# Optimization experiments

Hardware: AMD Instinct MI355X
Metric: run time of the kernel (lower is better)

Reference implementation:

```python
import jax, jax.numpy as jnp
import numpy as np

B, C, H, W = 8, 256, 128, 128
HEADS = 16
HEADC = C // HEADS  # 16
EPS = 1e-5


def setup_inputs() -> dict:
    key = jax.random.key(0)
    k1, k2 = jax.random.split(key)
    x = jax.random.normal(k1, (B, C, H, W), dtype=jnp.float32)
    w_qkv = jax.random.normal(k2, (3 * C, C), dtype=jnp.float32) * (1.0 / np.sqrt(C))
    b_qkv = jnp.zeros((3 * C,), dtype=jnp.float32)
    kln_w = jnp.ones((HEADS, HEADC), dtype=jnp.float32)
    kln_b = jnp.zeros((HEADS, HEADC), dtype=jnp.float32)
    vln_w = jnp.ones((HEADS, HEADC), dtype=jnp.float32)
    vln_b = jnp.zeros((HEADS, HEADC), dtype=jnp.float32)
    return {"x": x, "w_qkv": w_qkv, "b_qkv": b_qkv,
            "kln_w": kln_w, "kln_b": kln_b, "vln_w": vln_w, "vln_b": vln_b}


def _layernorm(x, w, b):
    # torch-style: unbiased std (ddof=1), divides by (std + eps), over last dim
    mean = jnp.mean(x, axis=-1, keepdims=True)
    std = jnp.std(x, axis=-1, keepdims=True, ddof=1)
    return (x - mean) / (std + EPS) * w + b


def reference(x, w_qkv, b_qkv, kln_w, kln_b, vln_w, vln_b):
    b, c, h, w = x.shape
    n = h * w
    # 1x1 conv == per-pixel matmul over channels
    qkv = jnp.einsum('bchw,oc->bhwo', x, w_qkv) + b_qkv  # (B,H,W,3C)
    qkv = qkv.reshape(b, n, HEADS, -1)                   # (B,N,16,3*headc)
    q, k, v = jnp.split(qkv, 3, axis=-1)                 # each (B,N,16,headc)
    k = _layernorm(k, kln_w, kln_b)
    v = _layernorm(v, vln_w, vln_b)
    # linear (Galerkin) attention: kv = k^T v / N, out = q @ kv
    kv = jnp.einsum('bnhd,bnhe->bhde', k, v) / n         # (B,16,headc,headc)
    out = jnp.einsum('bnhd,bhde->bnhe', q, kv)           # (B,N,16,headc)
    out = out.reshape(b, h, w, c).transpose(0, 3, 1, 2)  # (B,C,H,W)
    return out
```

## Files before the change

kernel.cpp:

```cpp
#include <hip/hip_runtime.h>

typedef unsigned short u16;
typedef unsigned int u32;
typedef __attribute__((ext_vector_type(8))) short short8;
typedef __attribute__((ext_vector_type(4))) float f32x4;

#define NPIX 16384
#define LNEPS 1e-5f

__device__ __forceinline__ float bf2f(u16 u) {
  union { u32 i; float f; } x; x.i = ((u32)u) << 16; return x.f;
}
__device__ __forceinline__ u16 f2bf(float f) {
  union { float f; u32 i; } x; x.f = f;
  u32 r = x.i + 0x7fffu + ((x.i >> 16) & 1u);
  return (u16)(r >> 16);
}
__device__ __forceinline__ void gload_lds16(const void* g, void* l) {
  __builtin_amdgcn_global_load_lds((__attribute__((address_space(1))) void*)(g),
                                   (__attribute__((address_space(3))) void*)(l),
                                   16, 0, 0);
}
__device__ __forceinline__ uint4 pack8(float4 a, float4 b) {
  uint4 q;
  q.x = (u32)f2bf(a.x) | ((u32)f2bf(a.y) << 16);
  q.y = (u32)f2bf(a.z) | ((u32)f2bf(a.w) << 16);
  q.z = (u32)f2bf(b.x) | ((u32)f2bf(b.y) << 16);
  q.w = (u32)f2bf(b.z) | ((u32)f2bf(b.w) << 16);
  return q;
}

__global__ __launch_bounds__(256) void k_detect(const u16* __restrict__ x,
                                                int* __restrict__ flag) {
  float mx = 0.f;
  for (int i = threadIdx.x; i < 4096; i += 256) {
    float v = fabsf(bf2f(x[2 * i]));
    if (v == v) mx = fmaxf(mx, v);
  }
  for (int m = 1; m < 64; m <<= 1) mx = fmaxf(mx, __shfl_xor(mx, m));
  __shared__ float wmax[4];
  if ((threadIdx.x & 63) == 0) wmax[threadIdx.x >> 6] = mx;
  __syncthreads();
  if (threadIdx.x == 0) {
    float m2 = fmaxf(fmaxf(wmax[0], wmax[1]), fmaxf(wmax[2], wmax[3]));
    flag[0] = (m2 > 1e5f) ? 1 : 0;
  }
}

__global__ __launch_bounds__(256) void k_wconv(
    const void* __restrict__ w, const void* __restrict__ bq,
    const void* __restrict__ klw, const void* __restrict__ klb,
    const void* __restrict__ vlw, const void* __restrict__ vlb,
    u16* __restrict__ wkv, u16* __restrict__ wq,
    float* __restrict__ bias_kv, float* __restrict__ lnw_kv,
    float* __restrict__ lnb_kv, float* __restrict__ bq_q,
    const int* __restrict__ flag) {
  const int i = blockIdx.x * 256 + threadIdx.x;
  const bool f32 = flag[0] != 0;
  auto getf = [&](const void* p, int j) -> float {
    return f32 ? ((const float*)p)[j] : bf2f(((const u16*)p)[j]);
  };
  if (i < 131072) {
    int o = i >> 8, c = i & 255;
    int h = o >> 5, tt = (o >> 4) & 1, d = o & 15;
    wkv[i] = f2bf(getf(w, (h * 48 + 16 + tt * 16 + d) * 256 + c));
  } else if (i < 196608) {
    int j = i - 131072; int r = j >> 8, c = j & 255;
    wq[j] = f2bf(getf(w, ((r >> 4) * 48 + (r & 15)) * 256 + c));
  } else if (i < 198400) {
    int j = i - 196608;
    if (j < 512) {
      int h = j >> 5, tt = (j >> 4) & 1, d = j & 15;
      bias_kv[j] = getf(bq, h * 48 + 16 + tt * 16 + d);
    } else if (j < 1024) {
      int o = j - 512; int h = o >> 5, tt = (o >> 4) & 1, d = o & 15;
      lnw_kv[o] = getf(tt ? vlw : klw, h * 16 + d);
    } else if (j < 1536) {
      int o = j - 1024; int h = o >> 5, tt = (o >> 4) & 1, d = o & 15;
      lnb_kv[o] = getf(tt ? vlb : klb, h * 16 + d);
    } else {
      int r = j - 1536;
      bq_q[r] = getf(bq, (r >> 4) * 48 + (r & 15));
    }
  }
}

__global__ __launch_bounds__(512, 4) void k_gemm1(
    const void* __restrict__ xin, const u16* __restrict__ wkv,
    const float* __restrict__ bias_kv, const float* __restrict__ lnw_kv,
    const float* __restrict__ lnb_kv, float* __restrict__ kvpart,
    const int* __restrict__ flag) {
  __shared__ alignas(16) char shraw[73728];
  u16 (*wlds)[256][32] = (u16 (*)[256][32])shraw;
  u16 (*xlds)[32][128] = (u16 (*)[32][128])(shraw + 32768);
  u16 (*klds)[260]     = (u16 (*)[260])shraw;
  float* bls = (float*)(shraw + 66560);
  float* wls = bls + 256;
  float* lls = bls + 512;
  float (*tmp)[256] = (float (*)[256])(shraw + 69632);

  const int t = threadIdx.x;
  const int lbid = ((blockIdx.x & 7) << 8) + (blockIdx.x >> 3);
  const int hg = lbid & 1;
  const int pc = (lbid >> 1) & 127;
  const int b  = lbid >> 8;
  const int p0 = pc * 128;
  const int wv = t >> 6, lane = t & 63, quad = lane >> 4, l16 = lane & 15;
  const int hl = wv & 1, pxq = wv >> 1;
  const bool f32 = flag[0] != 0;

  if (t < 256) {
    bls[t] = bias_kv[hg * 256 + t];
    wls[t] = lnw_kv[hg * 256 + t];
    lls[t] = lnb_kv[hg * 256 + t];
  }

  f32x4 acc[8][2];
#pragma unroll
  for (int ms = 0; ms < 8; ++ms) {
    acc[ms][0] = (f32x4){0.f, 0.f, 0.f, 0.f};
    acc[ms][1] = (f32x4){0.f, 0.f, 0.f, 0.f};
  }

  const int wrow = t >> 2;
  const int wcs  = t & 3;
  const int wks  = (wcs ^ ((t >> 3) & 3)) * 8;
  const u16* wsrc = wkv + ((size_t)(hg * 256 + wrow) * 256 + wks);

  const int xrow = t >> 4;
  const int xg   = (t & 15) ^ ((xrow >> 3) << 1);
  const u16* xsrc_bf = (const u16*)xin +
      ((size_t)(b * 256 + xrow) * NPIX + p0 + xg * 8);
  const float* xsrc_f = (const float*)xin +
      ((size_t)(b * 256 + xrow) * NPIX + p0 + xg * 8);

  gload_lds16(wsrc, &wlds[0][wrow][wcs * 8]);
  gload_lds16(wsrc + (size_t)128 * 256, &wlds[0][128 + wrow][wcs * 8]);
  if (!f32) {
    gload_lds16(xsrc_bf, &xlds[0][xrow][(t & 15) * 8]);
  } else {
    float4 a = *(const float4*)xsrc_f;
    float4 c = *(const float4*)(xsrc_f + 4);
    *(uint4*)&xlds[0][xrow][(t & 15) * 8] = pack8(a, c);
  }
  __syncthreads();

  for (int ks = 0; ks < 8; ++ks) {
    const int cur = ks & 1, nxt = cur ^ 1;
    const bool more = ks < 7;
    float4 v0, v1;
    if (more) {
      const u16* ws = wsrc + (ks + 1) * 32;
      gload_lds16(ws, &wlds[nxt][wrow][wcs * 8]);
      gload_lds16(ws + (size_t)128 * 256, &wlds[nxt][128 + wrow][wcs * 8]);
      if (!f32) {
        gload_lds16(xsrc_bf + (size_t)(ks + 1) * 32 * NPIX,
                    &xlds[nxt][xrow][(t & 15) * 8]);
      } else {
        const float* xf = xsrc_f + (size_t)(ks + 1) * 32 * NPIX;
        v0 = *(const float4*)xf;
        v1 = *(const float4*)(xf + 4);
      }
    }
    short8 bfr[2];
#pragma unroll
    for (int ns = 0; ns < 2; ++ns) {
      const int pxn = pxq * 32 + ns * 16 + l16;
      const int cs8 = ((((pxn >> 3) ^ (quad << 1)) << 3) + (pxn & 7));
      short8 bv;
#pragma unroll
      for (int j = 0; j < 8; ++j)
        bv[j] = (short)xlds[cur][quad * 8 + j][cs8];
      bfr[ns] = bv;
    }
#pragma unroll
    for (int ms = 0; ms < 8; ++ms) {
      const int row = hl * 128 + ms * 16 + l16;
      short8 av = *(const short8*)&wlds[cur][row][(quad ^ ((l16 >> 1) & 3)) * 8];
      acc[ms][0] = __builtin_amdgcn_mfma_f32_16x16x32_bf16(av, bfr[0], acc[ms][0], 0, 0, 0);
      acc[ms][1] = __builtin_amdgcn_mfma_f32_16x16x32_bf16(av, bfr[1], acc[ms][1], 0, 0, 0);
    }
    if (more && f32)
      *(uint4*)&xlds[nxt][xrow][(t & 15) * 8] = pack8(v0, v1);
    __syncthreads();
  }

#pragma unroll
  for (int p = 0; p < 2; ++p) {
    __syncthreads();
#pragma unroll
    for (int j = 0; j < 4; ++j) {
      const int msl = p * 4 + j;
      const int slot = (j >> 1) | (hl << 1);
      const int cb = slot * 64 + (j & 1) * 16;
      float4 bi = *(const float4*)&bls[hl * 128 + msl * 16 + quad * 4];
      float4 lw = *(const float4*)&wls[hl * 128 + msl * 16 + quad * 4];
      float4 lb = *(const float4*)&lls[hl * 128 + msl * 16 + quad * 4];
      float biv[4] = {bi.x, bi.y, bi.z, bi.w};
      float lwv[4] = {lw.x, lw.y, lw.z, lw.w};
      float lbv[4] = {lb.x, lb.y, lb.z, lb.w};
#pragma unroll
      for (int ns = 0; ns < 2; ++ns) {
        const int px = pxq * 32 + ns * 16 + l16;
        float x0[4];
#pragma unroll
        for (int r = 0; r < 4; ++r) x0[r] = acc[msl][ns][r] + biv[r];
        float s1 = x0[0] + x0[1] + x0[2] + x0[3];
        s1 += __shfl_xor(s1, 16);
        s1 += __shfl_xor(s1, 32);
        float mean = s1 * (1.0f / 16.0f);
        float dv[4];
#pragma unroll
        for (int r = 0; r < 4; ++r) dv[r] = x0[r] - mean;
        float s2 = dv[0]*dv[0] + dv[1]*dv[1] + dv[2]*dv[2] + dv[3]*dv[3];
        s2 += __shfl_xor(s2, 16);
        s2 += __shfl_xor(s2, 32);
        float var = s2 * (1.0f / 15.0f);
        float rstd = 1.0f / (sqrtf(var) + LNEPS);
        u16 hi[4], lo[4];
#pragma unroll
        for (int r = 0; r < 4; ++r) {
          float kn = dv[r] * rstd * lwv[r] + lbv[r];
          hi[r] = f2bf(kn);
          lo[r] = f2bf(kn - bf2f(hi[r]));
        }
        uint2 ph, pl;
        ph.x = (u32)hi[0] | ((u32)hi[1] << 16);
        ph.y = (u32)hi[2] | ((u32)hi[3] << 16);
        pl.x = (u32)lo[0] | ((u32)lo[1] << 16);
        pl.y = (u32)lo[2] | ((u32)lo[3] << 16);
        *(uint2*)&klds[px][cb + quad * 4] = ph;
        *(uint2*)&klds[px][cb + 32 + quad * 4] = pl;
      }
    }
    __syncthreads();
    const int slot4 = wv >> 1, combo = wv & 1;
    const int cb2 = slot4 * 64;
    f32x4 kva = (f32x4){0.f, 0.f, 0.f, 0.f};
    if (combo == 0) {
#pragma unroll
      for (int px2 = 0; px2 < 4; ++px2) {
        short8 av, bv;
#pragma unroll
        for (int jj = 0; jj < 8; ++jj) {
          av[jj] = (short)klds[px2 * 32 + quad * 8 + jj][cb2 + l16];
          bv[jj] = (short)klds[px2 * 32 + quad * 8 + jj][cb2 + 16 + l16];
        }
        kva = __builtin_amdgcn_mfma_f32_16x16x32_bf16(av, bv, kva, 0, 0, 0);
      }
    } else {
#pragma unroll
      for (int px2 = 0; px2 < 4; ++px2) {
        short8 ah, al, vh, vl;
#pragma unroll
        for (int jj = 0; jj < 8; ++jj) {
          const int px = px2 * 32 + quad * 8 + jj;
          ah[jj] = (short)klds[px][cb2 + l16];
          vh[jj] = (short)klds[px][cb2 + 16 + l16];
          al[jj] = (short)klds[px][cb2 + 32 + l16];
          vl[jj] = (short)klds[px][cb2 + 48 + l16];
        }
        kva = __builtin_amdgcn_mfma_f32_16x16x32_bf16(ah, vl, kva, 0, 0, 0);
        kva = __builtin_amdgcn_mfma_f32_16x16x32_bf16(al, vh, kva, 0, 0, 0);
      }
    }
    __syncthreads();
    if (combo) {
#pragma unroll
      for (int r = 0; r < 4; ++r) tmp[slot4][(quad * 4 + r) * 16 + l16] = kva[r];
    }
    __syncthreads();
    if (!combo) {
      const int h = (slot4 >> 1) * 4 + p * 2 + (slot4 & 1);
      float* kvp = kvpart +
          ((size_t)(((b * 128 + pc) * 2 + hg) * 8 + h) << 8);
#pragma unroll
      for (int r = 0; r < 4; ++r) {
        const int idx = (quad * 4 + r) * 16 + l16;
        kvp[idx] = kva[r] + tmp[slot4][idx];
      }
    }
  }
}

__global__ __launch_bounds__(256) void k_fold(const u16* __restrict__ wq,
                                              const float* __restrict__ bq_q,
                                              const float* __restrict__ kvpart,
                                              u16* __restrict__ whi,
                                              u16* __restrict__ wlo,
                                              float* __restrict__ beff) {
  __shared__ float kvs[256];
  __shared__ float qb[16];
  const int t = threadIdx.x;
  const int b = blockIdx.x >> 4, h = blockIdx.x & 15;
  const int hg = h >> 3, hl = h & 7;
  const float* src = kvpart + ((size_t)((b * 128 * 2 + hg) * 8 + hl) << 8) + t;
  float s0 = 0.f;
  for (int pc = 0; pc < 128; ++pc)
    s0 += src[(size_t)pc * (2 * 8 * 256)];
  kvs[t] = s0 * (1.0f / 16384.0f);
  if (t < 16) qb[t] = bq_q[h * 16 + t];
  __syncthreads();
  const int e = t >> 4, c0 = (t & 15) * 16;
  float o[16];
#pragma unroll
  for (int c = 0; c < 16; ++c) o[c] = 0.f;
  for (int d = 0; d < 16; ++d) {
    float kv_de = kvs[d * 16 + e];
    const u16* wr = wq + (size_t)(h * 16 + d) * 256 + c0;
#pragma unroll
    for (int c = 0; c < 16; ++c) o[c] = fmaf(bf2f(wr[c]), kv_de, o[c]);
  }
  const size_t wbase = (size_t)(b * 256 + h * 16 + e) * 256 + c0;
#pragma unroll
  for (int c = 0; c < 16; ++c) {
    u16 hi = f2bf(o[c]);
    whi[wbase + c] = hi;
    wlo[wbase + c] = f2bf(o[c] - bf2f(hi));
  }
  if (t < 16) {
    float s = 0.f;
    for (int d = 0; d < 16; ++d) s += qb[d] * kvs[d * 16 + t];
    beff[b * 256 + h * 16 + t] = s;
  }
}

__global__ __launch_bounds__(512, 4) void k_gemm2(
    const void* __restrict__ xin, const u16* __restrict__ whi,
    const u16* __restrict__ wlo, const float* __restrict__ beff,
    void* __restrict__ outv, const int* __restrict__ flag) {
  __shared__ u16 wldh[2][256][32];
  __shared__ u16 wldl[2][256][32];
  __shared__ u16 xlds[2][32][128];

  const int t = threadIdx.x;
  const int lbid = ((blockIdx.x & 7) << 7) + (blockIdx.x >> 3);
  const int pc = lbid & 127;
  const int b  = lbid >> 7;
  const int p0 = pc * 128;
  const int wv = t >> 6, lane = t & 63, quad = lane >> 4, l16 = lane & 15;
  const int hl = wv & 1, pxq = wv >> 1;
  const bool f32 = flag[0] != 0;

  f32x4 acc[8][2];
#pragma unroll
  for (int ms = 0; ms < 8; ++ms) {
    acc[ms][0] = (f32x4){0.f, 0.f, 0.f, 0.f};
    acc[ms][1] = (f32x4){0.f, 0.f, 0.f, 0.f};
  }

  const int wrow = t >> 2;
  const int wcs  = t & 3;
  const int wks  = (wcs ^ ((t >> 3) & 3)) * 8;
  const size_t wbase = (size_t)(b * 256 + wrow) * 256 + wks;
  const u16* wsrch = whi + wbase;
  const u16* wsrcl = wlo + wbase;

  const int xrow = t >> 4;
  const int xg   = (t & 15) ^ ((xrow >> 3) << 1);
  const u16* xsrc_bf = (const u16*)xin +
      ((size_t)(b * 256 + xrow) * NPIX + p0 + xg * 8);
  const float* xsrc_f = (const float*)xin +
      ((size_t)(b * 256 + xrow) * NPIX + p0 + xg * 8);

  gload_lds16(wsrch, &wldh[0][wrow][wcs * 8]);
  gload_lds16(wsrch + (size_t)128 * 256, &wldh[0][128 + wrow][wcs * 8]);
  gload_lds16(wsrcl, &wldl[0][wrow][wcs * 8]);
  gload_lds16(wsrcl + (size_t)128 * 256, &wldl[0][128 + wrow][wcs * 8]);
  if (!f32) {
    gload_lds16(xsrc_bf, &xlds[0][xrow][(t & 15) * 8]);
  } else {
    float4 a = *(const float4*)xsrc_f;
    float4 c = *(const float4*)(xsrc_f + 4);
    *(uint4*)&xlds[0][xrow][(t & 15) * 8] = pack8(a, c);
  }
  __syncthreads();

  for (int ks = 0; ks < 8; ++ks) {
    const int cur = ks & 1, nxt = cur ^ 1;
    const bool more = ks < 7;
    float4 v0, v1;
    if (more) {
      const u16* wh = wsrch + (ks + 1) * 32;
      const u16* wl = wsrcl + (ks + 1) * 32;
      gload_lds16(wh, &wldh[nxt][wrow][wcs * 8]);
      gload_lds16(wh + (size_t)128 * 256, &wldh[nxt][128 + wrow][wcs * 8]);
      gload_lds16(wl, &wldl[nxt][wrow][wcs * 8]);
      gload_lds16(wl + (size_t)128 * 256, &wldl[nxt][128 + wrow][wcs * 8]);
      if (!f32) {
        gload_lds16(xsrc_bf + (size_t)(ks + 1) * 32 * NPIX,
                    &xlds[nxt][xrow][(t & 15) * 8]);
      } else {
        const float* xf = xsrc_f + (size_t)(ks + 1) * 32 * NPIX;
        v0 = *(const float4*)xf;
        v1 = *(const float4*)(xf + 4);
      }
    }
    short8 bfr[2];
#pragma unroll
    for (int ns = 0; ns < 2; ++ns) {
      const int pxn = pxq * 32 + ns * 16 + l16;
      const int cs8 = ((((pxn >> 3) ^ (quad << 1)) << 3) + (pxn & 7));
      short8 bv;
#pragma unroll
      for (int j = 0; j < 8; ++j)
        bv[j] = (short)xlds[cur][quad * 8 + j][cs8];
      bfr[ns] = bv;
    }
#pragma unroll
    for (int ms = 0; ms < 8; ++ms) {
      const int row = hl * 128 + ms * 16 + l16;
      const int csw = (quad ^ ((l16 >> 1) & 3)) * 8;
      short8 avh = *(const short8*)&wldh[cur][row][csw];
      short8 avl = *(const short8*)&wldl[cur][row][csw];
      acc[ms][0] = __builtin_amdgcn_mfma_f32_16x16x32_bf16(avh, bfr[0], acc[ms][0], 0, 0, 0);
      acc[ms][0] = __builtin_amdgcn_mfma_f32_16x16x32_bf16(avl, bfr[0], acc[ms][0], 0, 0, 0);
      acc[ms][1] = __builtin_amdgcn_mfma_f32_16x16x32_bf16(avh, bfr[1], acc[ms][1], 0, 0, 0);
      acc[ms][1] = __builtin_amdgcn_mfma_f32_16x16x32_bf16(avl, bfr[1], acc[ms][1], 0, 0, 0);
    }
    if (more && f32)
      *(uint4*)&xlds[nxt][xrow][(t & 15) * 8] = pack8(v0, v1);
    __syncthreads();
  }

  const size_t obase = (size_t)b * 256 * NPIX + p0;
#pragma unroll
  for (int ms = 0; ms < 8; ++ms) {
    const int o0 = hl * 128 + ms * 16 + quad * 4;
    float4 be = *(const float4*)&beff[b * 256 + o0];
    float bev[4] = {be.x, be.y, be.z, be.w};
#pragma unroll
    for (int ns = 0; ns < 2; ++ns) {
      const int px = pxq * 32 + ns * 16 + l16;
#pragma unroll
      for (int r = 0; r < 4; ++r) {
        const int o = o0 + r;
        float val = acc[ms][ns][r] + bev[r];
        if (f32) ((float*)outv)[obase + (size_t)o * NPIX + px] = val;
        else ((u16*)outv)[obase + (size_t)o * NPIX + px] = f2bf(val);
      }
    }
  }
}

extern "C" void kernel_launch(void* const* d_in, const int* in_sizes, int n_in,
                              void* d_out, int out_size, void* d_ws, size_t ws_size,
                              hipStream_t stream) {
  (void)in_sizes; (void)n_in; (void)out_size; (void)ws_size;
  char* ws = (char*)d_ws;
  u16* wkv       = (u16*)(ws + 0);
  u16* wq        = (u16*)(ws + 262144);
  u16* weff_hi   = (u16*)(ws + 393216);
  u16* weff_lo   = (u16*)(ws + 1441792);
  float* bias_kv = (float*)(ws + 2621440);
  float* lnw_kv  = (float*)(ws + 2623488);
  float* lnb_kv  = (float*)(ws + 2625536);
  float* bq_q    = (float*)(ws + 2627584);
  float* beff    = (float*)(ws + 2628608);
  int* flag      = (int*)(ws + 2636800);
  float* kvpart  = (float*)(ws + 4194304);

  k_detect<<<1, 256, 0, stream>>>((const u16*)d_in[0], flag);
  k_wconv<<<775, 256, 0, stream>>>(d_in[1], d_in[2], d_in[3], d_in[4], d_in[5],
                                   d_in[6], wkv, wq, bias_kv, lnw_kv, lnb_kv,
                                   bq_q, flag);
  k_gemm1<<<2048, 512, 0, stream>>>(d_in[0], wkv, bias_kv, lnw_kv, lnb_kv,
                                    kvpart, flag);
  k_fold<<<128, 256, 0, stream>>>(wq, bq_q, kvpart, weff_hi, weff_lo, beff);
  k_gemm2<<<1024, 512, 0, stream>>>(d_in[0], weff_hi, weff_lo, beff, d_out, flag);
}
```

Measured before the change: 378.5 us.

## Triple-buffer GEMM1 LDS staging with prefetch distance two and partial waits

Replaces the double-buffered weight/input LDS staging in the K/V projection GEMM with a three-slot ring buffer that prefetches two k-steps ahead. It uses explicit s_waitcnt vmcnt(3) so the loads for the following step stay in flight across the barrier, and fully unrolls the k-loop. The goal is to hide global-to-LDS latency behind MFMA work. In exchange LDS use rises from about 72KB to 79KB per block, which may reduce how many blocks fit per CU, and the hand-written waitcnt counts depend on the exact number of outstanding loads.

```diff
diff --git a/kernel.cpp b/kernel.cpp
--- a/kernel.cpp
+++ b/kernel.cpp
@@ -90,14 +90,14 @@
     const float* __restrict__ bias_kv, const float* __restrict__ lnw_kv,
     const float* __restrict__ lnb_kv, float* __restrict__ kvpart,
     const int* __restrict__ flag) {
-  __shared__ alignas(16) char shraw[73728];
-  u16 (*wlds)[256][32] = (u16 (*)[256][32])shraw;
-  u16 (*xlds)[32][128] = (u16 (*)[32][128])(shraw + 32768);
-  u16 (*klds)[260]     = (u16 (*)[260])shraw;
-  float* bls = (float*)(shraw + 66560);
+  __shared__ alignas(16) char shraw[80896];
+  u16* wb0 = (u16*)shraw;
+  u16* xb0 = (u16*)(shraw + 49152);
+  u16 (*klds)[260] = (u16 (*)[260])shraw;
+  float* bls = (float*)(shraw + 73728);
   float* wls = bls + 256;
   float* lls = bls + 512;
-  float (*tmp)[256] = (float (*)[256])(shraw + 69632);
+  float (*tmp)[256] = (float (*)[256])(shraw + 76800);
 
   const int t = threadIdx.x;
   const int lbid = ((blockIdx.x & 7) << 8) + (blockIdx.x >> 3);
@@ -134,34 +134,34 @@
   const float* xsrc_f = (const float*)xin +
       ((size_t)(b * 256 + xrow) * NPIX + p0 + xg * 8);
 
-  gload_lds16(wsrc, &wlds[0][wrow][wcs * 8]);
-  gload_lds16(wsrc + (size_t)128 * 256, &wlds[0][128 + wrow][wcs * 8]);
-  if (!f32) {
-    gload_lds16(xsrc_bf, &xlds[0][xrow][(t & 15) * 8]);
-  } else {
-    float4 a = *(const float4*)xsrc_f;
-    float4 c = *(const float4*)(xsrc_f + 4);
-    *(uint4*)&xlds[0][xrow][(t & 15) * 8] = pack8(a, c);
-  }
-  __syncthreads();
-
+  auto STAGE = [&](int T, int B) {
+    const u16* ws = wsrc + T * 32;
+    gload_lds16(ws, wb0 + B * 8192 + wrow * 32 + wcs * 8);
+    gload_lds16(ws + (size_t)128 * 256,
+                wb0 + B * 8192 + (128 + wrow) * 32 + wcs * 8);
+    if (!f32) {
+      gload_lds16(xsrc_bf + (size_t)T * 32 * NPIX,
+                  xb0 + B * 4096 + xrow * 128 + (t & 15) * 8);
+    } else {
+      const float* xf = xsrc_f + (size_t)T * 32 * NPIX;
+      float4 a = *(const float4*)xf;
+      float4 c = *(const float4*)(xf + 4);
+      *(uint4*)(xb0 + B * 4096 + xrow * 128 + (t & 15) * 8) = pack8(a, c);
+    }
+  };
+
+  STAGE(0, 0);
+  STAGE(1, 1);
+  asm volatile("s_waitcnt vmcnt(0) lgkmcnt(0)" ::: "memory");
+  __builtin_amdgcn_s_barrier();
+  __builtin_amdgcn_sched_barrier(0);
+
+#pragma unroll
   for (int ks = 0; ks < 8; ++ks) {
-    const int cur = ks & 1, nxt = cur ^ 1;
-    const bool more = ks < 7;
-    float4 v0, v1;
-    if (more) {
-      const u16* ws = wsrc + (ks + 1) * 32;
-      gload_lds16(ws, &wlds[nxt][wrow][wcs * 8]);
-      gload_lds16(ws + (size_t)128 * 256, &wlds[nxt][128 + wrow][wcs * 8]);
-      if (!f32) {
-        gload_lds16(xsrc_bf + (size_t)(ks + 1) * 32 * NPIX,
-                    &xlds[nxt][xrow][(t & 15) * 8]);
-      } else {
-        const float* xf = xsrc_f + (size_t)(ks + 1) * 32 * NPIX;
-        v0 = *(const float4*)xf;
-        v1 = *(const float4*)(xf + 4);
-      }
-    }
+    const int cur = ks % 3;
+    if (ks < 6) STAGE(ks + 2, (ks + 2) % 3);
+    const u16* wlc = wb0 + cur * 8192;
+    const u16* xlc = xb0 + cur * 4096;
     short8 bfr[2];
 #pragma unroll
     for (int ns = 0; ns < 2; ++ns) {
@@ -170,19 +170,24 @@
       short8 bv;
 #pragma unroll
       for (int j = 0; j < 8; ++j)
-        bv[j] = (short)xlds[cur][quad * 8 + j][cs8];
+        bv[j] = (short)xlc[(quad * 8 + j) * 128 + cs8];
       bfr[ns] = bv;
     }
 #pragma unroll
     for (int ms = 0; ms < 8; ++ms) {
       const int row = hl * 128 + ms * 16 + l16;
-      short8 av = *(const short8*)&wlds[cur][row][(quad ^ ((l16 >> 1) & 3)) * 8];
+      short8 av = *(const short8*)(wlc + row * 32 + (quad ^ ((l16 >> 1) & 3)) * 8);
       acc[ms][0] = __builtin_amdgcn_mfma_f32_16x16x32_bf16(av, bfr[0], acc[ms][0], 0, 0, 0);
       acc[ms][1] = __builtin_amdgcn_mfma_f32_16x16x32_bf16(av, bfr[1], acc[ms][1], 0, 0, 0);
     }
-    if (more && f32)
-      *(uint4*)&xlds[nxt][xrow][(t & 15) * 8] = pack8(v0, v1);
-    __syncthreads();
+    if (!f32) {
+      if (ks < 6) asm volatile("s_waitcnt vmcnt(3) lgkmcnt(0)" ::: "memory");
+      else        asm volatile("s_waitcnt vmcnt(0) lgkmcnt(0)" ::: "memory");
+    } else {
+      asm volatile("s_waitcnt vmcnt(0) lgkmcnt(0)" ::: "memory");
+    }
+    __builtin_amdgcn_s_barrier();
+    __builtin_amdgcn_sched_barrier(0);
   }
 
 #pragma unroll
```

New measurement: 387.9 us. +2.5%, slower.
